# Kernel optimization log

Measured on AMD Instinct MI355X. Metric: run time of the kernel, lower is better.

## Reference

```python
import jax, jax.numpy as jnp
import numpy as np

B, I, S, H, O = 128, 64, 2048, 128, 64


def setup_inputs() -> dict:
    key = jax.random.key(0)
    ks = jax.random.split(key, 9)
    sc = 0.1
    return {
        "x": jax.random.normal(ks[0], (B, I, S), dtype=jnp.float32),
        "Wx_out": jax.random.normal(ks[1], (I, 4 * H), dtype=jnp.float32) * sc,
        "Wh_out": jax.random.normal(ks[2], (H, 4 * H), dtype=jnp.float32) * sc,
        "b_out": jnp.zeros((4 * H,), dtype=jnp.float32),
        "Wx_in": jax.random.normal(ks[3], (H, 4 * H), dtype=jnp.float32) * sc,
        "Wh_in": jax.random.normal(ks[4], (H, 4 * H), dtype=jnp.float32) * sc,
        "b_in": jnp.zeros((4 * H,), dtype=jnp.float32),
        "W_lin": jax.random.normal(ks[5], (O, H), dtype=jnp.float32) * 0.01,
        "b_lin": jnp.zeros((O,), dtype=jnp.float32),
    }


def reference(x, Wx_out, Wh_out, b_out, Wx_in, Wh_in, b_in, W_lin, b_lin):
    # x: (B, I, S) -> permute(0,2,1) -> (B, S, I); scan over time axis.
    xs = jnp.transpose(x, (2, 0, 1))  # (S, B, I)
    h0 = jnp.zeros((x.shape[0], Wh_out.shape[0]), dtype=x.dtype)

    def step(carry, xt):
        h, c, cn = carry  # outer hidden, outer cell, inner cell
        gates = xt @ Wx_out + h @ Wh_out + b_out
        i, f, o, g = jnp.split(gates, 4, axis=-1)
        i, f, o = jax.nn.sigmoid(i), jax.nn.sigmoid(f), jax.nn.sigmoid(o)
        g = jnp.tanh(g)
        x_in = i * g          # inner LSTM input
        h_in = f * c          # inner LSTM hidden
        gi = x_in @ Wx_in + h_in @ Wh_in + b_in
        ii, fi, oi, gg = jnp.split(gi, 4, axis=-1)
        cn_new = jax.nn.sigmoid(fi) * cn + jax.nn.sigmoid(ii) * jnp.tanh(gg)
        c_new = jax.nn.sigmoid(oi) * jnp.tanh(cn_new)  # outer cell = inner hidden
        h_new = o * jnp.tanh(c_new)
        return (h_new, c_new, cn_new), h_new

    _, hs = jax.lax.scan(step, (h0, h0, h0), xs)  # hs: (S, B, H)
    hs = jnp.transpose(hs, (1, 0, 2))             # (B, S, H)
    return hs @ W_lin.T + b_lin                   # (B, S, O)
```

## Files before the change

### kernel.cpp

```cpp
#include <hip/hip_runtime.h>
#include <hip/hip_fp16.h>

#define BB 128
#define II 64
#define SS 2048
#define HH 128
#define GG 512
#define OO 64

typedef _Float16 f16x2 __attribute__((ext_vector_type(2)));
union F4H { float4 f4; f16x2 h[4]; };

__device__ __forceinline__ f16x2 pack2(float a, float b) {
    f16x2 r; r.x = (_Float16)a; r.y = (_Float16)b; return r;
}

__device__ __forceinline__ float dot2(f16x2 w, f16x2 v, float c) {
#if __has_builtin(__builtin_amdgcn_fdot2)
    return __builtin_amdgcn_fdot2(w, v, c, false);
#else
    return fmaf((float)w.x, (float)v.x, fmaf((float)w.y, (float)v.y, c));
#endif
}

__device__ __forceinline__ float tanh_f(float v) {
    float a = fabsf(v);
    float e = __expf(-2.0f * a);
    float r = (1.0f - e) * __builtin_amdgcn_rcpf(1.0f + e);
    return v < 0.0f ? -r : r;
}

template<int C>
__device__ __forceinline__ float qb(float v) {
    return __int_as_float(__builtin_amdgcn_mov_dpp(
        __float_as_int(v), 0x55 * C, 0xF, 0xF, true));
}
template<int N>
__device__ __forceinline__ float rolN(float v) {
    return __int_as_float(__builtin_amdgcn_mov_dpp(
        __float_as_int(v), 0x120 + (16 - N), 0xF, 0xF, true));
}

__device__ __forceinline__ void barrier_lds() {
    asm volatile("s_waitcnt lgkmcnt(0)\n\ts_barrier" ::: "memory");
}

__global__ void __launch_bounds__(512)
nlstm_gatex(const float* __restrict__ x, const float* __restrict__ Wx_out,
            const float* __restrict__ b_out, float* __restrict__ gx,
            int t0, int nchunk)
{
    const int bb  = blockIdx.x / nchunk;
    const int tcw = blockIdx.x % nchunk;
    const int j   = threadIdx.x;
    const int u = j >> 2, g = j & 3;
    const int jcol = g * HH + u;

    __shared__ __align__(16) f16x2 xs[128][36];

    f16x2 wxo[II / 2];
#pragma unroll
    for (int m = 0; m < II / 2; ++m)
        wxo[m] = pack2(Wx_out[(2 * m) * GG + jcol],
                       Wx_out[(2 * m + 1) * GG + jcol]);
    const float bo = b_out[jcol];

    const float* xrow = x + (size_t)bb * II * SS;
    const int T0 = t0 + tcw * 128;
#pragma unroll
    for (int r = 0; r < 8; ++r) {
        const int idx = r * 512 + j;
        const int m = idx >> 7, tt = idx & 127;
        xs[tt][m] = pack2(xrow[(size_t)(2 * m) * SS + T0 + tt],
                          xrow[(size_t)(2 * m + 1) * SS + T0 + tt]);
    }
    __syncthreads();

#pragma unroll 1
    for (int tt = 0; tt < 128; ++tt) {
        const float4* xc4 = (const float4*)&xs[tt][0];
        float a0 = bo, a1 = 0.f, a2 = 0.f, a3 = 0.f;
#pragma unroll
        for (int c = 0; c < 8; ++c) {
            F4H xu; xu.f4 = xc4[c];
            a0 = dot2(wxo[4 * c + 0], xu.h[0], a0);
            a1 = dot2(wxo[4 * c + 1], xu.h[1], a1);
            a2 = dot2(wxo[4 * c + 2], xu.h[2], a2);
            a3 = dot2(wxo[4 * c + 3], xu.h[3], a3);
        }
        const float v = (a0 + a1) + (a2 + a3);
        const size_t tl = (size_t)tcw * 128 + tt;
        gx[((size_t)bb * nchunk * 128 + tl) * GG + j] = v;
    }
}

template<bool PROJ_IN>
__global__ void __launch_bounds__(512)
__attribute__((amdgpu_waves_per_eu(2)))
nlstm_scan_seg(
    const float* __restrict__ Wh_out,
    const float* __restrict__ Wx_in, const float* __restrict__ Wh_in,
    const float* __restrict__ b_in,
    const float* __restrict__ W_lin, const float* __restrict__ b_lin,
    const float* __restrict__ gx, float* __restrict__ out,
    f16x2* __restrict__ hws, f16x2* __restrict__ hst,
    float* __restrict__ cst, float* __restrict__ cnst,
    int t0, int t1, int Tc)
{
    const int b = blockIdx.x;
    const int j = threadIdx.x;
    const int u = j >> 2;
    const int g = j & 3;
    const int jcol = g * HH + u;

    __shared__ __align__(16) f16x2 hb[HH / 2];
    __shared__ __align__(16) f16x2 xib[HH / 2];
    __shared__ __align__(16) f16x2 hib[HH / 2];

    f16x2 who[HH / 2];
    f16x2 wxi[HH / 2];
    f16x2 whi[HH / 2];
#pragma unroll
    for (int m = 0; m < HH / 2; ++m)
        who[m] = pack2(Wh_out[(2 * m) * GG + jcol], Wh_out[(2 * m + 1) * GG + jcol]);
#pragma unroll
    for (int m = 0; m < HH / 2; ++m)
        wxi[m] = pack2(Wx_in[(2 * m) * GG + jcol], Wx_in[(2 * m + 1) * GG + jcol]);
#pragma unroll
    for (int m = 0; m < HH / 2; ++m)
        whi[m] = pack2(Wh_in[(2 * m) * GG + jcol], Wh_in[(2 * m + 1) * GG + jcol]);

    const float bi2 = b_in[jcol];

    const int   pn = j >> 3;
    const int   ps = j & 7;
    float bl = 0.f;
    F4H wl[2];
    if constexpr (PROJ_IN) {
        bl = b_lin[pn];
#pragma unroll
        for (int q = 0; q < 2; ++q) {
            const int c = 2 * ps + q;
#pragma unroll
            for (int r = 0; r < 4; ++r)
                wl[q].h[r] = pack2(W_lin[pn * HH + 8 * c + 2 * r],
                                   W_lin[pn * HH + 8 * c + 2 * r + 1]);
        }
    }

    float* orow = out + (size_t)b * SS * OO;
    f16x2* hrow = (PROJ_IN ? (f16x2*)nullptr : hws + (size_t)b * SS * (HH / 2));
    const float* gxrow = gx + (size_t)b * Tc * GG;

    float c_reg, cn_reg;
    if (t0 == 0) {
        if (j < HH / 2) hb[j] = pack2(0.f, 0.f);
        c_reg = 0.f; cn_reg = 0.f;
    } else {
        if (j < HH / 2) hb[j] = hst[b * (HH / 2) + j];
        c_reg  = cst[b * HH + u];
        cn_reg = cnst[b * HH + u];
    }
    __syncthreads();

    const float4* hb4 = (const float4*)hb;
    const float4* xi4 = (const float4*)xib;
    const float4* hi4 = (const float4*)hib;
    const bool isT = (g == 3);

    float gx_cur = gxrow[j];

#pragma unroll 1
    for (int t = t0; t < t1; ++t) {
        const int tl = t - t0;

        const int tln = (tl + 1 < Tc) ? tl + 1 : tl;
        const float gx_nxt = gxrow[(size_t)tln * GG + j];

        float a0 = gx_cur, a1 = 0.f, a2 = 0.f, a3 = 0.f;
#pragma unroll
        for (int c = 0; c < 16; ++c) {
            F4H hu; hu.f4 = hb4[c];
            a0 = dot2(who[4 * c + 0], hu.h[0], a0);
            a1 = dot2(who[4 * c + 1], hu.h[1], a1);
            a2 = dot2(who[4 * c + 2], hu.h[2], a2);
            a3 = dot2(who[4 * c + 3], hu.h[3], a3);
        }
        float acc = (a0 + a1) + (a2 + a3);

        float ap = isT ? 2.f * acc : acc;
        float s  = __builtin_amdgcn_rcpf(1.f + __expf(-ap));
        float av = isT ? fmaf(2.f, s, -1.f) : s;

        float vi = qb<0>(av), vf = qb<1>(av), vo = qb<2>(av), vg = qb<3>(av);
        float x_in    = vi * vg;
        float h_in    = vf * c_reg;
        float o_outer = vo;

        if constexpr (PROJ_IN) {
            float p0 = 0.f, p1 = 0.f;
            F4H hu0; hu0.f4 = hb4[2 * ps];
            F4H hu1; hu1.f4 = hb4[2 * ps + 1];
            p0 = dot2(wl[0].h[0], hu0.h[0], p0);
            p1 = dot2(wl[0].h[1], hu0.h[1], p1);
            p0 = dot2(wl[0].h[2], hu0.h[2], p0);
            p1 = dot2(wl[0].h[3], hu0.h[3], p1);
            p0 = dot2(wl[1].h[0], hu1.h[0], p0);
            p1 = dot2(wl[1].h[1], hu1.h[1], p1);
            p0 = dot2(wl[1].h[2], hu1.h[2], p0);
            p1 = dot2(wl[1].h[3], hu1.h[3], p1);
            float p = p0 + p1;
            p += rolN<4>(p);
            p += rolN<2>(p);
            p += rolN<1>(p);
            if (ps == 0 && t > 0) orow[(size_t)(t - 1) * OO + pn] = p + bl;
        }

        float xin_n = rolN<4>(x_in);
        float hin_n = rolN<4>(h_in);
        if ((j & 7) == 0) {
            xib[u >> 1] = pack2(x_in, xin_n);
            hib[u >> 1] = pack2(h_in, hin_n);
        }
        barrier_lds();

        float b0 = 0.f, b1 = 0.f, b2 = 0.f, b3 = 0.f;
#pragma unroll
        for (int c = 0; c < 16; ++c) {
            F4H xu; xu.f4 = xi4[c];
            b0 = dot2(wxi[4 * c + 0], xu.h[0], b0);
            b1 = dot2(wxi[4 * c + 1], xu.h[1], b1);
            b2 = dot2(wxi[4 * c + 2], xu.h[2], b2);
            b3 = dot2(wxi[4 * c + 3], xu.h[3], b3);
        }
#pragma unroll
        for (int c = 0; c < 16; ++c) {
            F4H hu; hu.f4 = hi4[c];
            b0 = dot2(whi[4 * c + 0], hu.h[0], b0);
            b1 = dot2(whi[4 * c + 1], hu.h[1], b1);
            b2 = dot2(whi[4 * c + 2], hu.h[2], b2);
            b3 = dot2(whi[4 * c + 3], hu.h[3], b3);
        }
        float acc2 = ((b0 + b1) + (b2 + b3)) + bi2;

        float ap2 = isT ? 2.f * acc2 : acc2;
        float s2  = __builtin_amdgcn_rcpf(1.f + __expf(-ap2));
        float av2 = isT ? fmaf(2.f, s2, -1.f) : s2;

        float ii = qb<0>(av2), fi = qb<1>(av2), oi = qb<2>(av2), gg = qb<3>(av2);
        float cn_new = fmaf(fi, cn_reg, ii * gg);
        cn_reg = cn_new;
        float c_new = oi * tanh_f(cn_new);
        c_reg = c_new;
        float h_new = o_outer * tanh_f(c_new);

        float hn_n = rolN<4>(h_new);
        if ((j & 7) == 0) {
            f16x2 hp = pack2(h_new, hn_n);
            hb[u >> 1] = hp;
            if constexpr (!PROJ_IN)
                hrow[(size_t)t * (HH / 2) + (j >> 3)] = hp;
        }
        gx_cur = gx_nxt;
        barrier_lds();
    }

    if (j < HH / 2) hst[b * (HH / 2) + j] = hb[j];
    if (g == 0) { cst[b * HH + u] = c_reg; cnst[b * HH + u] = cn_reg; }

    if constexpr (PROJ_IN) {
        if (t1 == SS) {
            float p0 = 0.f, p1 = 0.f;
            F4H hu0; hu0.f4 = hb4[2 * ps];
            F4H hu1; hu1.f4 = hb4[2 * ps + 1];
            p0 = dot2(wl[0].h[0], hu0.h[0], p0);
            p1 = dot2(wl[0].h[1], hu0.h[1], p1);
            p0 = dot2(wl[0].h[2], hu0.h[2], p0);
            p1 = dot2(wl[0].h[3], hu0.h[3], p1);
            p0 = dot2(wl[1].h[0], hu1.h[0], p0);
            p1 = dot2(wl[1].h[1], hu1.h[1], p1);
            p0 = dot2(wl[1].h[2], hu1.h[2], p0);
            p1 = dot2(wl[1].h[3], hu1.h[3], p1);
            float p = p0 + p1;
            p += rolN<4>(p);
            p += rolN<2>(p);
            p += rolN<1>(p);
            if (ps == 0) orow[(size_t)(SS - 1) * OO + pn] = p + bl;
        }
    }
}

__global__ void __launch_bounds__(512)
__attribute__((amdgpu_waves_per_eu(2)))
nlstm_fused(
    const float* __restrict__ x,
    const float* __restrict__ Wx_out, const float* __restrict__ Wh_out,
    const float* __restrict__ b_out,
    const float* __restrict__ Wx_in, const float* __restrict__ Wh_in,
    const float* __restrict__ b_in,
    const float* __restrict__ W_lin, const float* __restrict__ b_lin,
    float* __restrict__ out)
{
    const int b = blockIdx.x;
    const int j = threadIdx.x;
    const int u = j >> 2, g = j & 3;
    const int jcol = g * HH + u;

    __shared__ __align__(16) float4 wxf[8 * 512];
    __shared__ __align__(16) f16x2 xt[2][16][36];
    __shared__ __align__(16) f16x2 hb[HH / 2];
    __shared__ __align__(16) f16x2 xib[HH / 2];
    __shared__ __align__(16) f16x2 hib[HH / 2];

    f16x2 who[HH / 2], wxi[HH / 2], whi[HH / 2];
#pragma unroll
    for (int m = 0; m < HH / 2; ++m)
        who[m] = pack2(Wh_out[(2 * m) * GG + jcol], Wh_out[(2 * m + 1) * GG + jcol]);
#pragma unroll
    for (int m = 0; m < HH / 2; ++m)
        wxi[m] = pack2(Wx_in[(2 * m) * GG + jcol], Wx_in[(2 * m + 1) * GG + jcol]);
#pragma unroll
    for (int m = 0; m < HH / 2; ++m)
        whi[m] = pack2(Wh_in[(2 * m) * GG + jcol], Wh_in[(2 * m + 1) * GG + jcol]);

    const float bo = b_out[jcol];
    const float bi2 = b_in[jcol];
    const int pn = j >> 3, ps = j & 7;
    const float bl = b_lin[pn];
    F4H wl[2];
#pragma unroll
    for (int q = 0; q < 2; ++q) {
        const int c = 2 * ps + q;
#pragma unroll
        for (int r = 0; r < 4; ++r)
            wl[q].h[r] = pack2(W_lin[pn * HH + 8 * c + 2 * r],
                               W_lin[pn * HH + 8 * c + 2 * r + 1]);
    }
#pragma unroll
    for (int c = 0; c < 8; ++c) {
        F4H w4;
#pragma unroll
        for (int q = 0; q < 4; ++q)
            w4.h[q] = pack2(Wx_out[(8 * c + 2 * q) * GG + jcol],
                            Wx_out[(8 * c + 2 * q + 1) * GG + jcol]);
        wxf[c * 512 + j] = w4.f4;
    }

    const float* xrow = x + (size_t)b * II * SS;
    float* orow = out + (size_t)b * SS * OO;
    const int xm = j >> 4, xtl = j & 15;
    const float* xg0 = xrow + (size_t)(2 * xm) * SS + xtl;
    const float* xg1 = xrow + (size_t)(2 * xm + 1) * SS + xtl;

    xt[0][xtl][xm] = pack2(xg0[0], xg1[0]);
    if (j < HH / 2) hb[j] = pack2(0.f, 0.f);
    __syncthreads();

    float c_reg = 0.f, cn_reg = 0.f;
    const float4* hb4 = (const float4*)hb;
    const float4* xi4 = (const float4*)xib;
    const float4* hi4 = (const float4*)hib;
    const bool isT = (g == 3);
    float pr0 = 0.f, pr1 = 0.f;

#pragma unroll 1
    for (int t = 0; t < SS; ++t) {
        const int stl = t & 15;
        const int tb = (t >> 4) & 1;
        if (stl == 0) {
            const int Tn = (t + 16 < SS) ? t + 16 : t;
            pr0 = xg0[Tn];
            pr1 = xg1[Tn];
        }
        const float4* xc4 = (const float4*)&xt[tb][stl][0];
        float a0 = bo, a1 = 0.f, a2 = 0.f, a3 = 0.f;
#pragma unroll
        for (int c = 0; c < 8; ++c) {
            F4H xu; xu.f4 = xc4[c];
            F4H wu; wu.f4 = wxf[c * 512 + j];
            a0 = dot2(wu.h[0], xu.h[0], a0);
            a1 = dot2(wu.h[1], xu.h[1], a1);
            a2 = dot2(wu.h[2], xu.h[2], a2);
            a3 = dot2(wu.h[3], xu.h[3], a3);
        }
#pragma unroll
        for (int c = 0; c < 16; ++c) {
            F4H hu; hu.f4 = hb4[c];
            a0 = dot2(who[4 * c + 0], hu.h[0], a0);
            a1 = dot2(who[4 * c + 1], hu.h[1], a1);
            a2 = dot2(who[4 * c + 2], hu.h[2], a2);
            a3 = dot2(who[4 * c + 3], hu.h[3], a3);
        }
        float acc = (a0 + a1) + (a2 + a3);
        float ap = isT ? 2.f * acc : acc;
        float s = __builtin_amdgcn_rcpf(1.f + __expf(-ap));
        float av = isT ? fmaf(2.f, s, -1.f) : s;
        float vi = qb<0>(av), vf = qb<1>(av), vo = qb<2>(av), vg = qb<3>(av);
        float x_in = vi * vg, h_in = vf * c_reg, o_outer = vo;

        float p0 = 0.f, p1 = 0.f;
        {
            F4H hu0; hu0.f4 = hb4[2 * ps];
            F4H hu1; hu1.f4 = hb4[2 * ps + 1];
            p0 = dot2(wl[0].h[0], hu0.h[0], p0);
            p1 = dot2(wl[0].h[1], hu0.h[1], p1);
            p0 = dot2(wl[0].h[2], hu0.h[2], p0);
            p1 = dot2(wl[0].h[3], hu0.h[3], p1);
            p0 = dot2(wl[1].h[0], hu1.h[0], p0);
            p1 = dot2(wl[1].h[1], hu1.h[1], p1);
            p0 = dot2(wl[1].h[2], hu1.h[2], p0);
            p1 = dot2(wl[1].h[3], hu1.h[3], p1);
        }
        float p = p0 + p1;
        p += rolN<4>(p);
        p += rolN<2>(p);
        p += rolN<1>(p);
        if (ps == 0 && t > 0) orow[(size_t)(t - 1) * OO + pn] = p + bl;

        float xin_n = rolN<4>(x_in);
        float hin_n = rolN<4>(h_in);
        if ((j & 7) == 0) {
            xib[u >> 1] = pack2(x_in, xin_n);
            hib[u >> 1] = pack2(h_in, hin_n);
        }
        barrier_lds();

        float b0 = 0.f, b1 = 0.f, b2 = 0.f, b3 = 0.f;
#pragma unroll
        for (int c = 0; c < 16; ++c) {
            F4H xu; xu.f4 = xi4[c];
            b0 = dot2(wxi[4 * c + 0], xu.h[0], b0);
            b1 = dot2(wxi[4 * c + 1], xu.h[1], b1);
            b2 = dot2(wxi[4 * c + 2], xu.h[2], b2);
            b3 = dot2(wxi[4 * c + 3], xu.h[3], b3);
        }
#pragma unroll
        for (int c = 0; c < 16; ++c) {
            F4H hu; hu.f4 = hi4[c];
            b0 = dot2(whi[4 * c + 0], hu.h[0], b0);
            b1 = dot2(whi[4 * c + 1], hu.h[1], b1);
            b2 = dot2(whi[4 * c + 2], hu.h[2], b2);
            b3 = dot2(whi[4 * c + 3], hu.h[3], b3);
        }
        float acc2 = ((b0 + b1) + (b2 + b3)) + bi2;
        float ap2 = isT ? 2.f * acc2 : acc2;
        float s2 = __builtin_amdgcn_rcpf(1.f + __expf(-ap2));
        float av2 = isT ? fmaf(2.f, s2, -1.f) : s2;
        float ii = qb<0>(av2), fi = qb<1>(av2), oi = qb<2>(av2), gg = qb<3>(av2);
        float cn_new = fmaf(fi, cn_reg, ii * gg);
        cn_reg = cn_new;
        float c_new = oi * tanh_f(cn_new);
        c_reg = c_new;
        float h_new = o_outer * tanh_f(c_new);
        float hn_n = rolN<4>(h_new);
        if ((j & 7) == 0) hb[u >> 1] = pack2(h_new, hn_n);
        if (stl == 0) xt[tb ^ 1][xtl][xm] = pack2(pr0, pr1);
        barrier_lds();
    }
    {
        float p0 = 0.f, p1 = 0.f;
        F4H hu0; hu0.f4 = hb4[2 * ps];
        F4H hu1; hu1.f4 = hb4[2 * ps + 1];
        p0 = dot2(wl[0].h[0], hu0.h[0], p0);
        p1 = dot2(wl[0].h[1], hu0.h[1], p1);
        p0 = dot2(wl[0].h[2], hu0.h[2], p0);
        p1 = dot2(wl[0].h[3], hu0.h[3], p1);
        p0 = dot2(wl[1].h[0], hu1.h[0], p0);
        p1 = dot2(wl[1].h[1], hu1.h[1], p1);
        p0 = dot2(wl[1].h[2], hu1.h[2], p0);
        p1 = dot2(wl[1].h[3], hu1.h[3], p1);
        float p = p0 + p1;
        p += rolN<4>(p);
        p += rolN<2>(p);
        p += rolN<1>(p);
        if (ps == 0) orow[(size_t)(SS - 1) * OO + pn] = p + bl;
    }
}

__global__ void __launch_bounds__(256)
nlstm_proj(const f16x2* __restrict__ hws, const float* __restrict__ W_lin,
           const float* __restrict__ b_lin, float* __restrict__ out)
{
    const int n  = threadIdx.x & 63;
    const int rg = threadIdx.x >> 6;

    f16x2 wn[HH / 2];
#pragma unroll
    for (int k = 0; k < HH / 2; ++k)
        wn[k] = pack2(W_lin[n * HH + 2 * k], W_lin[n * HH + 2 * k + 1]);
    const float bl = b_lin[n];

    const size_t r0 = (size_t)blockIdx.x * 512 + (size_t)rg * 128;
#pragma unroll 1
    for (int rr = 0; rr < 128; ++rr) {
        const size_t r = r0 + rr;
        const float4* hr = (const float4*)(hws + r * (HH / 2));
        float p0 = 0.f, p1 = 0.f, p2 = 0.f, p3 = 0.f;
#pragma unroll
        for (int c = 0; c < 16; ++c) {
            F4H hu; hu.f4 = hr[c];
            p0 = dot2(wn[4 * c + 0], hu.h[0], p0);
            p1 = dot2(wn[4 * c + 1], hu.h[1], p1);
            p2 = dot2(wn[4 * c + 2], hu.h[2], p2);
            p3 = dot2(wn[4 * c + 3], hu.h[3], p3);
        }
        out[r * OO + n] = ((p0 + p1) + (p2 + p3)) + bl;
    }
}

extern "C" void kernel_launch(void* const* d_in, const int* in_sizes, int n_in,
                              void* d_out, int out_size, void* d_ws, size_t ws_size,
                              hipStream_t stream) {
    (void)in_sizes; (void)n_in; (void)out_size;
    const float* x      = (const float*)d_in[0];
    const float* Wx_out = (const float*)d_in[1];
    const float* Wh_out = (const float*)d_in[2];
    const float* b_out  = (const float*)d_in[3];
    const float* Wx_in  = (const float*)d_in[4];
    const float* Wh_in  = (const float*)d_in[5];
    const float* b_in   = (const float*)d_in[6];
    const float* W_lin  = (const float*)d_in[7];
    const float* b_lin  = (const float*)d_in[8];
    float* out = (float*)d_out;

    const size_t hws_b = (size_t)BB * SS * (HH / 2) * sizeof(f16x2);
    const size_t hst_b = (size_t)BB * (HH / 2) * sizeof(f16x2);
    const size_t cst_b = (size_t)BB * HH * sizeof(float);
    const int tcs[5] = {2048, 1024, 512, 256, 128};

    int Tc = 0;
    bool proj_out = false;
    if (d_ws != nullptr) {
        for (int i = 0; i < 5 && Tc == 0; ++i) {
            const size_t gxb = (size_t)BB * tcs[i] * GG * sizeof(float);
            if (ws_size >= hws_b + hst_b + 2 * cst_b + gxb) { Tc = tcs[i]; proj_out = true; }
        }
        for (int i = 0; i < 5 && Tc == 0; ++i) {
            const size_t gxb = (size_t)BB * tcs[i] * GG * sizeof(float);
            if (ws_size >= hst_b + 2 * cst_b + gxb) Tc = tcs[i];
        }
    }

    if (Tc != 0) {
        char* p = (char*)d_ws;
        f16x2* hws = nullptr;
        if (proj_out) { hws = (f16x2*)p; p += hws_b; }
        f16x2* hst = (f16x2*)p; p += hst_b;
        float* cst  = (float*)p; p += cst_b;
        float* cnst = (float*)p; p += cst_b;
        float* gx   = (float*)p;
        const int nchunk = Tc / 128;

        for (int t0 = 0; t0 < SS; t0 += Tc) {
            nlstm_gatex<<<dim3(BB * nchunk), dim3(512), 0, stream>>>(
                x, Wx_out, b_out, gx, t0, nchunk);
            if (proj_out)
                nlstm_scan_seg<false><<<dim3(BB), dim3(512), 0, stream>>>(
                    Wh_out, Wx_in, Wh_in, b_in, W_lin, b_lin, gx, out,
                    hws, hst, cst, cnst, t0, t0 + Tc, Tc);
            else
                nlstm_scan_seg<true><<<dim3(BB), dim3(512), 0, stream>>>(
                    Wh_out, Wx_in, Wh_in, b_in, W_lin, b_lin, gx, out,
                    nullptr, hst, cst, cnst, t0, t0 + Tc, Tc);
        }
        if (proj_out)
            nlstm_proj<<<dim3(512), dim3(256), 0, stream>>>(hws, W_lin, b_lin, out);
    } else {
        nlstm_fused<<<dim3(BB), dim3(512), 0, stream>>>(
            x, Wx_out, Wh_out, b_out, Wx_in, Wh_in, b_in, W_lin, b_lin, out);
    }
}
```

Measured before the change: 3.841 ms.

## Split K across the gate quad so each lane reads a quarter of LDS vectors

Reorganizes the recurrent matvecs so the four lanes of a quad share one hidden unit. Each lane covers a quarter of the K dimension for all four gate columns, instead of one column over the full K. Partial sums are combined with DPP quad permutes, and each lane then selects its own gate's total. The goal is to cut per-lane LDS float4 reads from 16 to 4 per matvec, reducing LDS bandwidth and latency on the serial per-step critical path. The cost is extra DPP reductions and selects, with the same register footprint for weights.

```diff
diff --git a/kernel.cpp b/kernel.cpp
--- a/kernel.cpp
+++ b/kernel.cpp
@@ -30,11 +30,13 @@
     return v < 0.0f ? -r : r;
 }
 
+template<int P>
+__device__ __forceinline__ float qp(float v) {
+    return __int_as_float(__builtin_amdgcn_mov_dpp(
+        __float_as_int(v), P, 0xF, 0xF, true));
+}
 template<int C>
-__device__ __forceinline__ float qb(float v) {
-    return __int_as_float(__builtin_amdgcn_mov_dpp(
-        __float_as_int(v), 0x55 * C, 0xF, 0xF, true));
-}
+__device__ __forceinline__ float qb(float v) { return qp<0x55 * C>(v); }
 template<int N>
 __device__ __forceinline__ float rolN(float v) {
     return __int_as_float(__builtin_amdgcn_mov_dpp(
@@ -117,18 +119,24 @@
     __shared__ __align__(16) f16x2 xib[HH / 2];
     __shared__ __align__(16) f16x2 hib[HH / 2];
 
-    f16x2 who[HH / 2];
-    f16x2 wxi[HH / 2];
-    f16x2 whi[HH / 2];
-#pragma unroll
-    for (int m = 0; m < HH / 2; ++m)
-        who[m] = pack2(Wh_out[(2 * m) * GG + jcol], Wh_out[(2 * m + 1) * GG + jcol]);
-#pragma unroll
-    for (int m = 0; m < HH / 2; ++m)
-        wxi[m] = pack2(Wx_in[(2 * m) * GG + jcol], Wx_in[(2 * m + 1) * GG + jcol]);
-#pragma unroll
-    for (int m = 0; m < HH / 2; ++m)
-        whi[m] = pack2(Wh_in[(2 * m) * GG + jcol], Wh_in[(2 * m + 1) * GG + jcol]);
+    f16x2 who[4][16];
+    f16x2 wxi[4][16];
+    f16x2 whi[4][16];
+#pragma unroll
+    for (int c = 0; c < 4; ++c)
+#pragma unroll
+        for (int c4 = 0; c4 < 4; ++c4)
+#pragma unroll
+            for (int e = 0; e < 4; ++e) {
+                const int k0 = 8 * (g + 4 * c4) + 2 * e;
+                const int cc = c * HH + u;
+                who[c][4 * c4 + e] = pack2(Wh_out[(size_t)k0 * GG + cc],
+                                           Wh_out[(size_t)(k0 + 1) * GG + cc]);
+                wxi[c][4 * c4 + e] = pack2(Wx_in[(size_t)k0 * GG + cc],
+                                           Wx_in[(size_t)(k0 + 1) * GG + cc]);
+                whi[c][4 * c4 + e] = pack2(Wh_in[(size_t)k0 * GG + cc],
+                                           Wh_in[(size_t)(k0 + 1) * GG + cc]);
+            }
 
     const float bi2 = b_in[jcol];
 
@@ -177,16 +185,25 @@
         const int tln = (tl + 1 < Tc) ? tl + 1 : tl;
         const float gx_nxt = gxrow[(size_t)tln * GG + j];
 
-        float a0 = gx_cur, a1 = 0.f, a2 = 0.f, a3 = 0.f;
-#pragma unroll
-        for (int c = 0; c < 16; ++c) {
-            F4H hu; hu.f4 = hb4[c];
-            a0 = dot2(who[4 * c + 0], hu.h[0], a0);
-            a1 = dot2(who[4 * c + 1], hu.h[1], a1);
-            a2 = dot2(who[4 * c + 2], hu.h[2], a2);
-            a3 = dot2(who[4 * c + 3], hu.h[3], a3);
-        }
-        float acc = (a0 + a1) + (a2 + a3);
+        float p0 = 0.f, p1 = 0.f, p2 = 0.f, p3 = 0.f;
+#pragma unroll
+        for (int c4 = 0; c4 < 4; ++c4) {
+            F4H hu; hu.f4 = hb4[g + 4 * c4];
+#pragma unroll
+            for (int e = 0; e < 4; ++e) {
+                p0 = dot2(who[0][4 * c4 + e], hu.h[e], p0);
+                p1 = dot2(who[1][4 * c4 + e], hu.h[e], p1);
+                p2 = dot2(who[2][4 * c4 + e], hu.h[e], p2);
+                p3 = dot2(who[3][4 * c4 + e], hu.h[e], p3);
+            }
+        }
+        p0 += qp<0xB1>(p0); p1 += qp<0xB1>(p1);
+        p2 += qp<0xB1>(p2); p3 += qp<0xB1>(p3);
+        p0 += qp<0x4E>(p0); p1 += qp<0x4E>(p1);
+        p2 += qp<0x4E>(p2); p3 += qp<0x4E>(p3);
+        const float totO = (g & 1) ? ((g & 2) ? p3 : p1)
+                                   : ((g & 2) ? p2 : p0);
+        float acc = totO + gx_cur;
 
         float ap = isT ? 2.f * acc : acc;
         float s  = __builtin_amdgcn_rcpf(1.f + __expf(-ap));
@@ -198,18 +215,18 @@
         float o_outer = vo;
 
         if constexpr (PROJ_IN) {
-            float p0 = 0.f, p1 = 0.f;
+            float q0 = 0.f, q1 = 0.f;
             F4H hu0; hu0.f4 = hb4[2 * ps];
             F4H hu1; hu1.f4 = hb4[2 * ps + 1];
-            p0 = dot2(wl[0].h[0], hu0.h[0], p0);
-            p1 = dot2(wl[0].h[1], hu0.h[1], p1);
-            p0 = dot2(wl[0].h[2], hu0.h[2], p0);
-            p1 = dot2(wl[0].h[3], hu0.h[3], p1);
-            p0 = dot2(wl[1].h[0], hu1.h[0], p0);
-            p1 = dot2(wl[1].h[1], hu1.h[1], p1);
-            p0 = dot2(wl[1].h[2], hu1.h[2], p0);
-            p1 = dot2(wl[1].h[3], hu1.h[3], p1);
-            float p = p0 + p1;
+            q0 = dot2(wl[0].h[0], hu0.h[0], q0);
+            q1 = dot2(wl[0].h[1], hu0.h[1], q1);
+            q0 = dot2(wl[0].h[2], hu0.h[2], q0);
+            q1 = dot2(wl[0].h[3], hu0.h[3], q1);
+            q0 = dot2(wl[1].h[0], hu1.h[0], q0);
+            q1 = dot2(wl[1].h[1], hu1.h[1], q1);
+            q0 = dot2(wl[1].h[2], hu1.h[2], q0);
+            q1 = dot2(wl[1].h[3], hu1.h[3], q1);
+            float p = q0 + q1;
             p += rolN<4>(p);
             p += rolN<2>(p);
             p += rolN<1>(p);
@@ -224,28 +241,40 @@
         }
         barrier_lds();
 
-        float b0 = 0.f, b1 = 0.f, b2 = 0.f, b3 = 0.f;
-#pragma unroll
-        for (int c = 0; c < 16; ++c) {
-            F4H xu; xu.f4 = xi4[c];
-            b0 = dot2(wxi[4 * c + 0], xu.h[0], b0);
-            b1 = dot2(wxi[4 * c + 1], xu.h[1], b1);
-            b2 = dot2(wxi[4 * c + 2], xu.h[2], b2);
-            b3 = dot2(wxi[4 * c + 3], xu.h[3], b3);
-        }
-#pragma unroll
-        for (int c = 0; c < 16; ++c) {
-            F4H hu; hu.f4 = hi4[c];
-            b0 = dot2(whi[4 * c + 0], hu.h[0], b0);
-            b1 = dot2(whi[4 * c + 1], hu.h[1], b1);
-            b2 = dot2(whi[4 * c + 2], hu.h[2], b2);
-            b3 = dot2(whi[4 * c + 3], hu.h[3], b3);
-        }
-        float acc2 = ((b0 + b1) + (b2 + b3)) + bi2;
+        float s0 = 0.f, s1 = 0.f, s2 = 0.f, s3 = 0.f;
+#pragma unroll
+        for (int c4 = 0; c4 < 4; ++c4) {
+            F4H xu; xu.f4 = xi4[g + 4 * c4];
+#pragma unroll
+            for (int e = 0; e < 4; ++e) {
+                s0 = dot2(wxi[0][4 * c4 + e], xu.h[e], s0);
+                s1 = dot2(wxi[1][4 * c4 + e], xu.h[e], s1);
+                s2 = dot2(wxi[2][4 * c4 + e], xu.h[e], s2);
+                s3 = dot2(wxi[3][4 * c4 + e], xu.h[e], s3);
+            }
+        }
+#pragma unroll
+        for (int c4 = 0; c4 < 4; ++c4) {
+            F4H hu2; hu2.f4 = hi4[g + 4 * c4];
+#pragma unroll
+            for (int e = 0; e < 4; ++e) {
+                s0 = dot2(whi[0][4 * c4 + e], hu2.h[e], s0);
+                s1 = dot2(whi[1][4 * c4 + e], hu2.h[e], s1);
+                s2 = dot2(whi[2][4 * c4 + e], hu2.h[e], s2);
+                s3 = dot2(whi[3][4 * c4 + e], hu2.h[e], s3);
+            }
+        }
+        s0 += qp<0xB1>(s0); s1 += qp<0xB1>(s1);
+        s2 += qp<0xB1>(s2); s3 += qp<0xB1>(s3);
+        s0 += qp<0x4E>(s0); s1 += qp<0x4E>(s1);
+        s2 += qp<0x4E>(s2); s3 += qp<0x4E>(s3);
+        const float totI = (g & 1) ? ((g & 2) ? s3 : s1)
+                                   : ((g & 2) ? s2 : s0);
+        float acc2 = totI + bi2;
 
         float ap2 = isT ? 2.f * acc2 : acc2;
-        float s2  = __builtin_amdgcn_rcpf(1.f + __expf(-ap2));
-        float av2 = isT ? fmaf(2.f, s2, -1.f) : s2;
+        float s2a = __builtin_amdgcn_rcpf(1.f + __expf(-ap2));
+        float av2 = isT ? fmaf(2.f, s2a, -1.f) : s2a;
 
         float ii = qb<0>(av2), fi = qb<1>(av2), oi = qb<2>(av2), gg = qb<3>(av2);
         float cn_new = fmaf(fi, cn_reg, ii * gg);
@@ -270,18 +299,18 @@
 
     if constexpr (PROJ_IN) {
         if (t1 == SS) {
-            float p0 = 0.f, p1 = 0.f;
+            float q0 = 0.f, q1 = 0.f;
             F4H hu0; hu0.f4 = hb4[2 * ps];
             F4H hu1; hu1.f4 = hb4[2 * ps + 1];
-            p0 = dot2(wl[0].h[0], hu0.h[0], p0);
-            p1 = dot2(wl[0].h[1], hu0.h[1], p1);
-            p0 = dot2(wl[0].h[2], hu0.h[2], p0);
-            p1 = dot2(wl[0].h[3], hu0.h[3], p1);
-            p0 = dot2(wl[1].h[0], hu1.h[0], p0);
-            p1 = dot2(wl[1].h[1], hu1.h[1], p1);
-            p0 = dot2(wl[1].h[2], hu1.h[2], p0);
-            p1 = dot2(wl[1].h[3], hu1.h[3], p1);
-            float p = p0 + p1;
+            q0 = dot2(wl[0].h[0], hu0.h[0], q0);
+            q1 = dot2(wl[0].h[1], hu0.h[1], q1);
+            q0 = dot2(wl[0].h[2], hu0.h[2], q0);
+            q1 = dot2(wl[0].h[3], hu0.h[3], q1);
+            q0 = dot2(wl[1].h[0], hu1.h[0], q0);
+            q1 = dot2(wl[1].h[1], hu1.h[1], q1);
+            q0 = dot2(wl[1].h[2], hu1.h[2], q0);
+            q1 = dot2(wl[1].h[3], hu1.h[3], q1);
+            float p = q0 + q1;
             p += rolN<4>(p);
             p += rolN<2>(p);
             p += rolN<1>(p);
```

Result: faster. 3.577 ms (-6.9%).
